# Kernel tuning notes

Measured on AMD Instinct MI355X. Metric: run time of the kernel, lower is better.

Reference implementation:

```python
import jax, jax.numpy as jnp
import numpy as np

H = 16  # num_attention_heads
D = 64  # attention_head_size


def setup_inputs() -> dict:
    key = jax.random.key(0)
    ks = jax.random.split(key, 10)
    B, S, Hid = 8, 512, 1024
    scale = 0.02
    hidden_states = jax.random.normal(ks[0], (B, S, Hid), jnp.float32)
    attention_mask = jnp.zeros((B, 1, 1, S), jnp.float32)
    graph_emb = jax.random.randint(ks[1], (B, S, S), 0, 3, jnp.int32)
    Wq = jax.random.normal(ks[2], (Hid, Hid), jnp.float32) * scale
    bq = jnp.zeros((Hid,), jnp.float32)
    Wk = jax.random.normal(ks[3], (Hid, Hid), jnp.float32) * scale
    bk = jnp.zeros((Hid,), jnp.float32)
    Wv = jax.random.normal(ks[4], (Hid, Hid), jnp.float32) * scale
    bv = jnp.zeros((Hid,), jnp.float32)
    dp_k = jax.random.normal(ks[5], (3, D), jnp.float32) * scale
    dp_v = jax.random.normal(ks[6], (3, D), jnp.float32) * scale
    return {"hidden_states": hidden_states, "attention_mask": attention_mask,
            "graph_emb": graph_emb, "Wq": Wq, "bq": bq, "Wk": Wk, "bk": bk,
            "Wv": Wv, "bv": bv, "dp_k": dp_k, "dp_v": dp_v}


def reference(hidden_states, attention_mask, graph_emb, Wq, bq, Wk, bk, Wv, bv, dp_k, dp_v):
    B, S, Hid = hidden_states.shape

    def proj(W, b):  # nn.Linear: x @ W.T + b, then split heads -> [B,H,S,D]
        y = hidden_states @ W.T + b
        return y.reshape(B, S, H, D).transpose(0, 2, 1, 3)

    q = proj(Wq, bq)
    k = proj(Wk, bk)
    v = proj(Wv, bv)

    # padding_idx=0 -> row 0 of relation tables is zero
    dp_k = dp_k.at[0].set(0.0)
    dp_v = dp_v.at[0].set(0.0)
    dp_keys = dp_k[graph_emb]    # [B,S,S,D]
    dp_values = dp_v[graph_emb]  # [B,S,S,D]

    scores = jnp.einsum('bhqd,bhkd->bhqk', q, k) / jnp.sqrt(jnp.float32(D))
    scores = scores + jnp.einsum('bhqd,bqkd->bhqk', q, dp_keys)  # relative_matmul_dp
    scores = scores + attention_mask
    probs = jax.nn.softmax(scores, axis=-1)

    ctx = jnp.einsum('bhqk,bhkd->bhqd', probs, v)
    ctx = ctx + jnp.einsum('bhqk,bqkd->bhqd', probs, dp_values)  # relative_matmul_dpv
    return ctx.transpose(0, 2, 1, 3).reshape(B, S, H * D)
```

## Files before the change

### kernel.cpp

```cpp
#include <hip/hip_runtime.h>
#include <hip/hip_bf16.h>
#include <cstddef>

#define B_  8
#define S_  512
#define HID 1024
#define H_  16
#define D_  64

typedef float f32x4 __attribute__((ext_vector_type(4)));
typedef _Float16 f16x8 __attribute__((ext_vector_type(8)));
typedef short s16x8 __attribute__((ext_vector_type(8)));
typedef unsigned short u16t;

__device__ __forceinline__ u16t f2h(float v) {
    return __builtin_bit_cast(u16t, (_Float16)v);
}

__device__ __forceinline__ void gll16(const u16t* g, u16t* l) {
    __builtin_amdgcn_global_load_lds(
        (const __attribute__((address_space(1))) unsigned int*)(const void*)g,
        (__attribute__((address_space(3))) unsigned int*)(void*)l, 16, 0, 0);
}

#define WAITV4() asm volatile("s_waitcnt vmcnt(4)" ::: "memory")
#define WAITV0() asm volatile("s_waitcnt vmcnt(0)" ::: "memory")

__global__ __launch_bounds__(256) void conv_all_kernel(
    const float* __restrict__ X,
    const float* __restrict__ Wq, const float* __restrict__ Wk,
    const float* __restrict__ Wv,
    u16t* __restrict__ Xh, u16t* __restrict__ Wh)
{
    const int nX4 = (B_ * S_ * HID) / 4;
    const int nW4 = (HID * HID) / 4;
    int i = blockIdx.x * 256 + threadIdx.x;
    const float* src;
    u16t* dst;
    int off;
    if (i < nX4)                { src = X;  dst = Xh;                         off = i; }
    else if (i < nX4 + nW4)     { src = Wq; dst = Wh;                         off = i - nX4; }
    else if (i < nX4 + 2 * nW4) { src = Wk; dst = Wh + (size_t)HID * HID;     off = i - nX4 - nW4; }
    else                        { src = Wv; dst = Wh + (size_t)2 * HID * HID; off = i - nX4 - 2 * nW4; }
    float4 x = ((const float4*)src)[off];
    ushort4 h;
    h.x = f2h(x.x);
    h.y = f2h(x.y);
    h.z = f2h(x.z);
    h.w = f2h(x.w);
    ((ushort4*)dst)[off] = h;
}

__global__ __launch_bounds__(256) void pack_ge_kernel(
    const int* __restrict__ ge, unsigned char* __restrict__ ge8, int n4)
{
    int i = blockIdx.x * 256 + threadIdx.x;
    if (i >= n4) return;
    int4 v = ((const int4*)ge)[i];
    uchar4 p;
    p.x = (unsigned char)v.x;
    p.y = (unsigned char)v.y;
    p.z = (unsigned char)v.z;
    p.w = (unsigned char)v.w;
    ((uchar4*)ge8)[i] = p;
}

__global__ __launch_bounds__(256) void qkv_mfma_kernel(
    const u16t* __restrict__ Xhi, const u16t* __restrict__ Whi,
    const float* __restrict__ bq, const float* __restrict__ bk,
    const float* __restrict__ bv,
    u16t* __restrict__ Qh, u16t* __restrict__ Kh, u16t* __restrict__ Vth)
{
    const int which = blockIdx.z;
    const u16t* __restrict__ WhiB = Whi + (size_t)which * (HID * HID);
    const float* __restrict__ bias = (which == 0) ? bq : (which == 1) ? bk : bv;

    __shared__ __align__(16) u16t SM[24576];

    const int tid  = threadIdx.x;
    const int lane = tid & 63;
    const int wv_  = tid >> 6;
    const int wr   = wv_ >> 1;
    const int wc   = wv_ & 1;
    const int m0   = blockIdx.y * 128;
    const int n0   = blockIdx.x * 128;
    const int NT   = HID / 32;

    f32x4 acc[4][4];
    #pragma unroll
    for (int mi = 0; mi < 4; ++mi)
        #pragma unroll
        for (int ni = 0; ni < 4; ++ni)
            #pragma unroll
            for (int e = 0; e < 4; ++e) acc[mi][ni][e] = 0.0f;

    const int c0 = tid, c1 = 256 + tid;
    const int rp0 = c0 >> 3, u0 = (c0 & 7) ^ (rp0 & 7);
    const int rp1 = c1 >> 3, u1 = (c1 & 7) ^ (rp1 & 7);
    const size_t ga0 = (size_t)(m0 + 2 * rp0 + (u0 >> 2)) * HID + (u0 & 3) * 8;
    const size_t ga1 = (size_t)(m0 + 2 * rp1 + (u1 >> 2)) * HID + (u1 & 3) * 8;
    const size_t gb0 = (size_t)(n0 + 2 * rp0 + (u0 >> 2)) * HID + (u0 & 3) * 8;
    const size_t gb1 = (size_t)(n0 + 2 * rp1 + (u1 >> 2)) * HID + (u1 & 3) * 8;
    const int lA0 = wv_ * 512;
    const int lA1 = 2048 + wv_ * 512;

    const int colL = lane & 15;
    const int kg   = lane >> 4;
    int aoffR[4], boffR[4];
    #pragma unroll
    for (int mi = 0; mi < 4; ++mi) {
        const int mrow = wr * 64 + mi * 16 + colL;
        const int rp = mrow >> 1, hf = mrow & 1;
        aoffR[mi] = rp * 64 + ((((hf << 2) | kg) ^ (rp & 7)) << 3);
        const int nrow = wc * 64 + mi * 16 + colL;
        const int rq = nrow >> 1, hg = nrow & 1;
        boffR[mi] = rq * 64 + ((((hg << 2) | kg) ^ (rq & 7)) << 3);
    }

    #define STAGE_T(t) do {                                      \
        u16t* bb_ = SM + ((t) % 3) * 8192;                       \
        const size_t ko_ = (size_t)(t) * 32;                     \
        gll16(&Xhi [ga0 + ko_], bb_ + lA0);                      \
        gll16(&Xhi [ga1 + ko_], bb_ + lA1);                      \
        gll16(&WhiB[gb0 + ko_], bb_ + 4096 + lA0);               \
        gll16(&WhiB[gb1 + ko_], bb_ + 4096 + lA1);               \
    } while (0)

    STAGE_T(0);
    STAGE_T(1);

    for (int t = 0; t < NT; ++t) {
        if (t < NT - 1) WAITV4();
        else            WAITV0();
        __builtin_amdgcn_s_barrier();
        if (t + 2 < NT) STAGE_T(t + 2);

        u16t* const bc = SM + (t % 3) * 8192;
        f16x8 a_[4], b_[4];
        #pragma unroll
        for (int mi = 0; mi < 4; ++mi)
            a_[mi] = *(const f16x8*)&bc[aoffR[mi]];
        #pragma unroll
        for (int ni = 0; ni < 4; ++ni)
            b_[ni] = *(const f16x8*)&bc[4096 + boffR[ni]];
        #pragma unroll
        for (int mi = 0; mi < 4; ++mi)
            #pragma unroll
            for (int ni = 0; ni < 4; ++ni)
                acc[mi][ni] = __builtin_amdgcn_mfma_f32_16x16x32_f16(
                    a_[mi], b_[ni], acc[mi][ni], 0, 0, 0);
    }
    #undef STAGE_T

    if (which == 2) {
        #pragma unroll
        for (int mi = 0; mi < 4; ++mi) {
            #pragma unroll
            for (int ni = 0; ni < 4; ++ni) {
                const int n    = n0 + wc * 64 + ni * 16 + colL;
                const int mrow = m0 + wr * 64 + mi * 16 + kg * 4;
                const float bn = bias[n];
                const int bb = mrow >> 9;
                const int ss = mrow & (S_ - 1);
                const int hh = n >> 6;
                const int dd = n & (D_ - 1);
                ushort4 vh;
                vh.x = f2h(acc[mi][ni][0] + bn);
                vh.y = f2h(acc[mi][ni][1] + bn);
                vh.z = f2h(acc[mi][ni][2] + bn);
                vh.w = f2h(acc[mi][ni][3] + bn);
                *(ushort4*)&Vth[(((size_t)bb * H_ + hh) * D_ + dd) * S_ + ss] = vh;
            }
        }
    } else {
        u16t* __restrict__ Oh = (which == 0) ? Qh : Kh;
        float* LF = (float*)SM;
        float bn4[4];
        #pragma unroll
        for (int ni = 0; ni < 4; ++ni) bn4[ni] = bias[n0 + wc * 64 + ni * 16 + colL];

        const int er  = tid >> 3;
        const int ecc = (tid & 7) * 16;
        const int ehh = (n0 + ecc) >> 6;
        const int edd = ecc & 63;
        const int mrowE = m0 + (er >> 4) * 64 + (er & 15);

        #pragma unroll
        for (int mi = 0; mi < 4; ++mi) {
            __syncthreads();
            #pragma unroll
            for (int ni = 0; ni < 4; ++ni)
                #pragma unroll
                for (int j = 0; j < 4; ++j)
                    LF[(wr * 16 + kg * 4 + j) * 130 + wc * 64 + ni * 16 + colL] =
                        acc[mi][ni][j] + bn4[ni];
            __syncthreads();

            const int mrow = mrowE + mi * 16;
            const int bb = mrow >> 9;
            const int ss = mrow & (S_ - 1);
            __align__(16) u16t hv[16];
            #pragma unroll
            for (int u = 0; u < 16; u += 4) {
                float4 v = *(const float4*)&LF[er * 130 + ecc + u];
                hv[u + 0] = f2h(v.x);
                hv[u + 1] = f2h(v.y);
                hv[u + 2] = f2h(v.z);
                hv[u + 3] = f2h(v.w);
            }
            const size_t off = (((size_t)bb * H_ + ehh) * S_ + ss) * D_ + edd;
            *(s16x8*)&Oh[off]     = *(const s16x8*)&hv[0];
            *(s16x8*)&Oh[off + 8] = *(const s16x8*)&hv[8];
        }
    }
}

__global__ __launch_bounds__(512) void attn_mfma_kernel(
    const u16t* __restrict__ Qhg, const u16t* __restrict__ Khg,
    const u16t* __restrict__ Vhg,
    const unsigned char* __restrict__ ge8, const float* __restrict__ mask,
    const float* __restrict__ dpk, const float* __restrict__ dpv,
    float* __restrict__ out)
{
    __shared__ __align__(16) u16t SM[24576];

    const int tid  = threadIdx.x;
    const int lane = tid & 63;
    const int wq   = tid >> 6;
    const int c    = lane & 15;
    const int g    = lane >> 4;
    const int sx   = c & 7;
    const int bid  = blockIdx.x;
    const int bh   = bid >> 2;
    const int q0   = (bid & 3) * 128;
    const int b    = bh >> 4;
    const int h    = bh & (H_ - 1);

    u16t* Pw = SM + 16384 + wq * 1024;

    const int qrow = q0 + wq * 16 + c;
    const size_t qoff = ((size_t)bh * S_ + qrow) * D_;
    const f16x8 qA = *(const f16x8*)&Qhg[qoff + g * 8];
    const f16x8 qB = *(const f16x8*)&Qhg[qoff + (g + 4) * 8];

    float tq1, tq2;
    {
        float a1 = 0.f, a2 = 0.f;
        #pragma unroll
        for (int i = 0; i < 8; ++i) {
            const float x0 = (float)qA[i];
            const float x1 = (float)qB[i];
            a1 = fmaf(x0, dpk[D_ + g * 8 + i], a1);
            a1 = fmaf(x1, dpk[D_ + (g + 4) * 8 + i], a1);
            a2 = fmaf(x0, dpk[2 * D_ + g * 8 + i], a2);
            a2 = fmaf(x1, dpk[2 * D_ + (g + 4) * 8 + i], a2);
        }
        a1 += __shfl_xor(a1, 16); a1 += __shfl_xor(a1, 32);
        a2 += __shfl_xor(a2, 16); a2 += __shfl_xor(a2, 32);
        tq1 = a1; tq2 = a2;
    }

    const int r_   = tid >> 3;
    const int s_   = tid & 7;
    const int ldso = r_ * 64 + ((s_ ^ (r_ & 7)) << 3);
    const u16t* kgp = &Khg[((size_t)bh * S_ + r_) * D_ + s_ * 8];
    const u16t* vgp = &Vhg[((size_t)bh * D_ + r_) * S_ + s_ * 8];

    s16x8 krS = *(const s16x8*)kgp;
    s16x8 vrS = *(const s16x8*)vgp;

    const size_t geoff = ((size_t)b * S_ + qrow) * S_;
    const float* mrow = &mask[(size_t)b * S_];

    float lrun = 0.f, w1 = 0.f, w2 = 0.f;
    f32x4 ctx4[4];
    #pragma unroll
    for (int mi = 0; mi < 4; ++mi)
        #pragma unroll
        for (int e = 0; e < 4; ++e) ctx4[mi][e] = 0.f;

    for (int kt = 0; kt < S_ / 64; ++kt) {
        const int k0 = kt * 64;
        const int bufo = (kt & 1) << 13;
        u16t* const Kb = SM + bufo;
        u16t* const Vb = SM + bufo + 4096;

        *(s16x8*)&Kb[ldso] = krS;
        *(s16x8*)&Vb[ldso] = vrS;

        if (kt < S_ / 64 - 1) {
            krS = *(const s16x8*)(kgp + (size_t)(k0 + 64) * D_);
            vrS = *(const s16x8*)(vgp + (k0 + 64));
        }
        uchar4 gc4[4];
        float4 mk4[4];
        #pragma unroll
        for (int mi = 0; mi < 4; ++mi) {
            gc4[mi] = *(const uchar4*)&ge8[geoff + k0 + mi * 16 + g * 4];
            mk4[mi] = *(const float4*)&mrow[k0 + mi * 16 + g * 4];
        }

        __syncthreads();

        f32x4 s4[4];
        #pragma unroll
        for (int mi = 0; mi < 4; ++mi)
            #pragma unroll
            for (int e = 0; e < 4; ++e) s4[mi][e] = 0.f;

        __builtin_amdgcn_s_setprio(1);
        #pragma unroll
        for (int ks = 0; ks < 2; ++ks) {
            const int so = ((g + 4 * ks) ^ sx) << 3;
            const f16x8 qh_ = ks ? qB : qA;
            #pragma unroll
            for (int mi = 0; mi < 4; ++mi) {
                const f16x8 kh_ = *(const f16x8*)&Kb[(mi * 16 + c) * 64 + so];
                s4[mi] = __builtin_amdgcn_mfma_f32_16x16x32_f16(kh_, qh_, s4[mi], 0, 0, 0);
            }
        }
        __builtin_amdgcn_s_setprio(0);

        float sv[4][4];
        float rs = 0.f, rb1 = 0.f, rb2 = 0.f;
        #pragma unroll
        for (int mi = 0; mi < 4; ++mi) {
            const int   gg[4] = {gc4[mi].x, gc4[mi].y, gc4[mi].z, gc4[mi].w};
            const float mm[4] = {mk4[mi].x, mk4[mi].y, mk4[mi].z, mk4[mi].w};
            #pragma unroll
            for (int j = 0; j < 4; ++j) {
                const float t = (gg[j] == 1) ? tq1 : (gg[j] == 2) ? tq2 : 0.f;
                const float e = __expf(fmaf(s4[mi][j], 0.125f, t + mm[j] - 8.0f));
                sv[mi][j] = e;
                rs += e;
                rb1 += (gg[j] == 1) ? e : 0.f;
                rb2 += (gg[j] == 2) ? e : 0.f;
            }
        }
        rs  += __shfl_xor(rs, 16);  rs  += __shfl_xor(rs, 32);
        rb1 += __shfl_xor(rb1, 16); rb1 += __shfl_xor(rb1, 32);
        rb2 += __shfl_xor(rb2, 16); rb2 += __shfl_xor(rb2, 32);
        lrun += rs;
        w1   += rb1;
        w2   += rb2;

        #pragma unroll
        for (int mi = 0; mi < 4; ++mi) {
            ushort4 ph;
            ph.x = f2h(sv[mi][0]);
            ph.y = f2h(sv[mi][1]);
            ph.z = f2h(sv[mi][2]);
            ph.w = f2h(sv[mi][3]);
            const int slotp = (2 * mi + (g >> 1)) ^ sx;
            *(ushort4*)&Pw[c * 64 + slotp * 8 + (g & 1) * 4] = ph;
        }

        __builtin_amdgcn_s_setprio(1);
        #pragma unroll
        for (int ks = 0; ks < 2; ++ks) {
            const int so = ((g + 4 * ks) ^ sx) << 3;
            const f16x8 ph_ = *(const f16x8*)&Pw[c * 64 + so];
            #pragma unroll
            for (int mi = 0; mi < 4; ++mi) {
                const f16x8 vh_ = *(const f16x8*)&Vb[(mi * 16 + c) * 64 + so];
                ctx4[mi] = __builtin_amdgcn_mfma_f32_16x16x32_f16(vh_, ph_, ctx4[mi], 0, 0, 0);
            }
        }
        __builtin_amdgcn_s_setprio(0);
    }

    __syncthreads();
    const float inv = 1.0f / lrun;
    float* tb = (float*)SM + wq * 1088;
    #pragma unroll
    for (int mi = 0; mi < 4; ++mi) {
        const float4 dk1 = *(const float4*)&dpv[D_ + mi * 16 + g * 4];
        const float4 dk2 = *(const float4*)&dpv[2 * D_ + mi * 16 + g * 4];
        const float a1[4] = {dk1.x, dk1.y, dk1.z, dk1.w};
        const float a2[4] = {dk2.x, dk2.y, dk2.z, dk2.w};
        #pragma unroll
        for (int j = 0; j < 4; ++j) {
            const float val = (ctx4[mi][j] + w1 * a1[j] + w2 * a2[j]) * inv;
            tb[(mi * 16 + g * 4 + j) * 17 + c] = val;
        }
    }
    __syncthreads();
    #pragma unroll
    for (int qq = 0; qq < 16; ++qq)
        out[((size_t)b * S_ + q0 + wq * 16 + qq) * (H_ * D_) + h * D_ + lane] =
            tb[lane * 17 + qq];
}

extern "C" void kernel_launch(void* const* d_in, const int* in_sizes, int n_in,
                              void* d_out, int out_size, void* d_ws, size_t ws_size,
                              hipStream_t stream)
{
    const float* hs   = (const float*)d_in[0];
    const float* mask = (const float*)d_in[1];
    const int*   ge   = (const int*)d_in[2];
    const float* Wq   = (const float*)d_in[3];
    const float* bq   = (const float*)d_in[4];
    const float* Wk   = (const float*)d_in[5];
    const float* bk   = (const float*)d_in[6];
    const float* Wv   = (const float*)d_in[7];
    const float* bv   = (const float*)d_in[8];
    const float* dpk  = (const float*)d_in[9];
    const float* dpv  = (const float*)d_in[10];
    float* out = (float*)d_out;

    const size_t per = (size_t)B_ * H_ * S_ * D_;
    const size_t nX  = (size_t)B_ * S_ * HID;
    const size_t nW  = (size_t)HID * HID;
    const size_t nGe = (size_t)B_ * S_ * S_;

    u16t* base = (u16t*)d_ws;
    u16t* Qh  = base;
    u16t* Kh  = Qh  + per;
    u16t* Vth = Kh  + per;
    u16t* Xhi = Vth + per;
    u16t* Whi = Xhi + nX;
    unsigned char* ge8 = (unsigned char*)(Whi + 3 * nW);

    const int nConv = (int)((nX + 3 * nW) / 4);
    conv_all_kernel<<<nConv / 256, 256, 0, stream>>>(hs, Wq, Wk, Wv, Xhi, Whi);
    pack_ge_kernel<<<(int)(nGe / 4 / 256), 256, 0, stream>>>(ge, ge8, (int)(nGe / 4));

    dim3 gridG(HID / 128, (B_ * S_) / 128, 3);
    qkv_mfma_kernel<<<gridG, dim3(256), 0, stream>>>(
        Xhi, Whi, bq, bk, bv, Qh, Kh, Vth);

    dim3 gridB(B_ * H_ * (S_ / 128));
    attn_mfma_kernel<<<gridB, dim3(512), 0, stream>>>(
        Qh, Kh, Vth, ge8, mask, dpk, dpv, out);
}
```

Measured before the change: 84.54 us.

## Fuse Q/K/V projections into one GEMM block and drop graph-emb packing kernel

The QKV projection kernel now computes all three projections in one block, staging the shared X tile once and three weight tiles per k-step. Three accumulator sets are kept, and the grid shrinks from 3 slices to 1. This reuses the X loads across Q, K and V, but it triples accumulator registers (launch bounds set to 1 block), doubles LDS use and leaves far fewer blocks (256) to fill the GPU. Separately, the int8 pack kernel for graph_emb is removed and the attention kernel reads the int32 indices directly, saving a launch and a pass at the cost of 4x wider index loads inside attention.

```diff
diff --git a/kernel.cpp b/kernel.cpp
--- a/kernel.cpp
+++ b/kernel.cpp
@@ -23,7 +23,7 @@
         (__attribute__((address_space(3))) unsigned int*)(void*)l, 16, 0, 0);
 }
 
-#define WAITV4() asm volatile("s_waitcnt vmcnt(4)" ::: "memory")
+#define WAITV8() asm volatile("s_waitcnt vmcnt(8)" ::: "memory")
 #define WAITV0() asm volatile("s_waitcnt vmcnt(0)" ::: "memory")
 
 __global__ __launch_bounds__(256) void conv_all_kernel(
@@ -51,31 +51,17 @@
     ((ushort4*)dst)[off] = h;
 }
 
-__global__ __launch_bounds__(256) void pack_ge_kernel(
-    const int* __restrict__ ge, unsigned char* __restrict__ ge8, int n4)
-{
-    int i = blockIdx.x * 256 + threadIdx.x;
-    if (i >= n4) return;
-    int4 v = ((const int4*)ge)[i];
-    uchar4 p;
-    p.x = (unsigned char)v.x;
-    p.y = (unsigned char)v.y;
-    p.z = (unsigned char)v.z;
-    p.w = (unsigned char)v.w;
-    ((uchar4*)ge8)[i] = p;
-}
-
-__global__ __launch_bounds__(256) void qkv_mfma_kernel(
+__global__ __launch_bounds__(256, 1) void qkv_mfma_kernel(
     const u16t* __restrict__ Xhi, const u16t* __restrict__ Whi,
     const float* __restrict__ bq, const float* __restrict__ bk,
     const float* __restrict__ bv,
     u16t* __restrict__ Qh, u16t* __restrict__ Kh, u16t* __restrict__ Vth)
 {
-    const int which = blockIdx.z;
-    const u16t* __restrict__ WhiB = Whi + (size_t)which * (HID * HID);
-    const float* __restrict__ bias = (which == 0) ? bq : (which == 1) ? bk : bv;
-
-    __shared__ __align__(16) u16t SM[24576];
+    const u16t* __restrict__ Wh0 = Whi;
+    const u16t* __restrict__ Wh1 = Whi + (size_t)(HID * HID);
+    const u16t* __restrict__ Wh2 = Whi + (size_t)2 * (HID * HID);
+
+    __shared__ __align__(16) u16t SM[49152];
 
     const int tid  = threadIdx.x;
     const int lane = tid & 63;
@@ -86,13 +72,15 @@
     const int n0   = blockIdx.x * 128;
     const int NT   = HID / 32;
 
-    f32x4 acc[4][4];
+    f32x4 acc[3][4][4];
     #pragma unroll
-    for (int mi = 0; mi < 4; ++mi)
-        #pragma unroll
-        for (int ni = 0; ni < 4; ++ni)
-            #pragma unroll
-            for (int e = 0; e < 4; ++e) acc[mi][ni][e] = 0.0f;
+    for (int w = 0; w < 3; ++w)
+        #pragma unroll
+        for (int mi = 0; mi < 4; ++mi)
+            #pragma unroll
+            for (int ni = 0; ni < 4; ++ni)
+                #pragma unroll
+                for (int e = 0; e < 4; ++e) acc[w][mi][ni][e] = 0.0f;
 
     const int c0 = tid, c1 = 256 + tid;
     const int rp0 = c0 >> 3, u0 = (c0 & 7) ^ (rp0 & 7);
@@ -118,99 +106,111 @@
     }
 
     #define STAGE_T(t) do {                                      \
-        u16t* bb_ = SM + ((t) % 3) * 8192;                       \
+        u16t* bb_ = SM + ((t) % 3) * 16384;                      \
         const size_t ko_ = (size_t)(t) * 32;                     \
-        gll16(&Xhi [ga0 + ko_], bb_ + lA0);                      \
-        gll16(&Xhi [ga1 + ko_], bb_ + lA1);                      \
-        gll16(&WhiB[gb0 + ko_], bb_ + 4096 + lA0);               \
-        gll16(&WhiB[gb1 + ko_], bb_ + 4096 + lA1);               \
+        gll16(&Xhi[ga0 + ko_], bb_ + lA0);                       \
+        gll16(&Xhi[ga1 + ko_], bb_ + lA1);                       \
+        gll16(&Wh0[gb0 + ko_], bb_ + 4096  + lA0);               \
+        gll16(&Wh0[gb1 + ko_], bb_ + 4096  + lA1);               \
+        gll16(&Wh1[gb0 + ko_], bb_ + 8192  + lA0);               \
+        gll16(&Wh1[gb1 + ko_], bb_ + 8192  + lA1);               \
+        gll16(&Wh2[gb0 + ko_], bb_ + 12288 + lA0);               \
+        gll16(&Wh2[gb1 + ko_], bb_ + 12288 + lA1);               \
     } while (0)
 
     STAGE_T(0);
     STAGE_T(1);
 
     for (int t = 0; t < NT; ++t) {
-        if (t < NT - 1) WAITV4();
+        if (t < NT - 1) WAITV8();
         else            WAITV0();
         __builtin_amdgcn_s_barrier();
         if (t + 2 < NT) STAGE_T(t + 2);
 
-        u16t* const bc = SM + (t % 3) * 8192;
-        f16x8 a_[4], b_[4];
+        u16t* const bc = SM + (t % 3) * 16384;
+        f16x8 a_[4];
         #pragma unroll
         for (int mi = 0; mi < 4; ++mi)
             a_[mi] = *(const f16x8*)&bc[aoffR[mi]];
         #pragma unroll
-        for (int ni = 0; ni < 4; ++ni)
-            b_[ni] = *(const f16x8*)&bc[4096 + boffR[ni]];
-        #pragma unroll
-        for (int mi = 0; mi < 4; ++mi)
+        for (int w = 0; w < 3; ++w) {
+            f16x8 b_[4];
             #pragma unroll
             for (int ni = 0; ni < 4; ++ni)
-                acc[mi][ni] = __builtin_amdgcn_mfma_f32_16x16x32_f16(
-                    a_[mi], b_[ni], acc[mi][ni], 0, 0, 0);
+                b_[ni] = *(const f16x8*)&bc[4096 * (w + 1) + boffR[ni]];
+            #pragma unroll
+            for (int mi = 0; mi < 4; ++mi)
+                #pragma unroll
+                for (int ni = 0; ni < 4; ++ni)
+                    acc[w][mi][ni] = __builtin_amdgcn_mfma_f32_16x16x32_f16(
+                        a_[mi], b_[ni], acc[w][mi][ni], 0, 0, 0);
+        }
     }
     #undef STAGE_T
 
-    if (which == 2) {
+    {
+        float* LF = (float*)SM;
+        const int er  = tid >> 3;
+        const int ecc = (tid & 7) * 16;
+        const int ehh = (n0 + ecc) >> 6;
+        const int edd = ecc & 63;
+        const int mrowE = m0 + (er >> 4) * 64 + (er & 15);
+
+        #pragma unroll
+        for (int w = 0; w < 2; ++w) {
+            const float* __restrict__ bias = (w == 0) ? bq : bk;
+            u16t* __restrict__ Oh = (w == 0) ? Qh : Kh;
+            float bn4[4];
+            #pragma unroll
+            for (int ni = 0; ni < 4; ++ni) bn4[ni] = bias[n0 + wc * 64 + ni * 16 + colL];
+
+            #pragma unroll
+            for (int mi = 0; mi < 4; ++mi) {
+                __syncthreads();
+                #pragma unroll
+                for (int ni = 0; ni < 4; ++ni)
+                    #pragma unroll
+                    for (int j = 0; j < 4; ++j)
+                        LF[(wr * 16 + kg * 4 + j) * 130 + wc * 64 + ni * 16 + colL] =
+                            acc[w][mi][ni][j] + bn4[ni];
+                __syncthreads();
+
+                const int mrow = mrowE + mi * 16;
+                const int bb = mrow >> 9;
+                const int ss = mrow & (S_ - 1);
+                __align__(16) u16t hv[16];
+                #pragma unroll
+                for (int u = 0; u < 16; u += 4) {
+                    float4 v = *(const float4*)&LF[er * 130 + ecc + u];
+                    hv[u + 0] = f2h(v.x);
+                    hv[u + 1] = f2h(v.y);
+                    hv[u + 2] = f2h(v.z);
+                    hv[u + 3] = f2h(v.w);
+                }
+                const size_t off = (((size_t)bb * H_ + ehh) * S_ + ss) * D_ + edd;
+                *(s16x8*)&Oh[off]     = *(const s16x8*)&hv[0];
+                *(s16x8*)&Oh[off + 8] = *(const s16x8*)&hv[8];
+            }
+        }
+
         #pragma unroll
         for (int mi = 0; mi < 4; ++mi) {
             #pragma unroll
             for (int ni = 0; ni < 4; ++ni) {
                 const int n    = n0 + wc * 64 + ni * 16 + colL;
                 const int mrow = m0 + wr * 64 + mi * 16 + kg * 4;
-                const float bn = bias[n];
+                const float bn = bv[n];
                 const int bb = mrow >> 9;
                 const int ss = mrow & (S_ - 1);
                 const int hh = n >> 6;
                 const int dd = n & (D_ - 1);
                 ushort4 vh;
-                vh.x = f2h(acc[mi][ni][0] + bn);
-                vh.y = f2h(acc[mi][ni][1] + bn);
-                vh.z = f2h(acc[mi][ni][2] + bn);
-                vh.w = f2h(acc[mi][ni][3] + bn);
+                vh.x = f2h(acc[2][mi][ni][0] + bn);
+                vh.y = f2h(acc[2][mi][ni][1] + bn);
+                vh.z = f2h(acc[2][mi][ni][2] + bn);
+                vh.w = f2h(acc[2][mi][ni][3] + bn);
                 *(ushort4*)&Vth[(((size_t)bb * H_ + hh) * D_ + dd) * S_ + ss] = vh;
             }
-        }
-    } else {
-        u16t* __restrict__ Oh = (which == 0) ? Qh : Kh;
-        float* LF = (float*)SM;
-        float bn4[4];
-        #pragma unroll
-        for (int ni = 0; ni < 4; ++ni) bn4[ni] = bias[n0 + wc * 64 + ni * 16 + colL];
-
-        const int er  = tid >> 3;
-        const int ecc = (tid & 7) * 16;
-        const int ehh = (n0 + ecc) >> 6;
-        const int edd = ecc & 63;
-        const int mrowE = m0 + (er >> 4) * 64 + (er & 15);
-
-        #pragma unroll
-        for (int mi = 0; mi < 4; ++mi) {
-            __syncthreads();
-            #pragma unroll
-            for (int ni = 0; ni < 4; ++ni)
-                #pragma unroll
-                for (int j = 0; j < 4; ++j)
-                    LF[(wr * 16 + kg * 4 + j) * 130 + wc * 64 + ni * 16 + colL] =
-                        acc[mi][ni][j] + bn4[ni];
-            __syncthreads();
-
-            const int mrow = mrowE + mi * 16;
-            const int bb = mrow >> 9;
-            const int ss = mrow & (S_ - 1);
-            __align__(16) u16t hv[16];
-            #pragma unroll
-            for (int u = 0; u < 16; u += 4) {
-                float4 v = *(const float4*)&LF[er * 130 + ecc + u];
-                hv[u + 0] = f2h(v.x);
-                hv[u + 1] = f2h(v.y);
-                hv[u + 2] = f2h(v.z);
-                hv[u + 3] = f2h(v.w);
-            }
-            const size_t off = (((size_t)bb * H_ + ehh) * S_ + ss) * D_ + edd;
-            *(s16x8*)&Oh[off]     = *(const s16x8*)&hv[0];
-            *(s16x8*)&Oh[off + 8] = *(const s16x8*)&hv[8];
         }
     }
 }
@@ -218,7 +218,7 @@
 __global__ __launch_bounds__(512) void attn_mfma_kernel(
     const u16t* __restrict__ Qhg, const u16t* __restrict__ Khg,
     const u16t* __restrict__ Vhg,
-    const unsigned char* __restrict__ ge8, const float* __restrict__ mask,
+    const int*  __restrict__ ge,  const float* __restrict__ mask,
     const float* __restrict__ dpk, const float* __restrict__ dpv,
     float* __restrict__ out)
 {
@@ -292,11 +292,11 @@
             krS = *(const s16x8*)(kgp + (size_t)(k0 + 64) * D_);
             vrS = *(const s16x8*)(vgp + (k0 + 64));
         }
-        uchar4 gc4[4];
+        int4   gc4[4];
         float4 mk4[4];
         #pragma unroll
         for (int mi = 0; mi < 4; ++mi) {
-            gc4[mi] = *(const uchar4*)&ge8[geoff + k0 + mi * 16 + g * 4];
+            gc4[mi] = *(const int4*)&ge[geoff + k0 + mi * 16 + g * 4];
             mk4[mi] = *(const float4*)&mrow[k0 + mi * 16 + g * 4];
         }
 
@@ -411,7 +411,6 @@
     const size_t per = (size_t)B_ * H_ * S_ * D_;
     const size_t nX  = (size_t)B_ * S_ * HID;
     const size_t nW  = (size_t)HID * HID;
-    const size_t nGe = (size_t)B_ * S_ * S_;
 
     u16t* base = (u16t*)d_ws;
     u16t* Qh  = base;
@@ -419,17 +418,15 @@
     u16t* Vth = Kh  + per;
     u16t* Xhi = Vth + per;
     u16t* Whi = Xhi + nX;
-    unsigned char* ge8 = (unsigned char*)(Whi + 3 * nW);
 
     const int nConv = (int)((nX + 3 * nW) / 4);
     conv_all_kernel<<<nConv / 256, 256, 0, stream>>>(hs, Wq, Wk, Wv, Xhi, Whi);
-    pack_ge_kernel<<<(int)(nGe / 4 / 256), 256, 0, stream>>>(ge, ge8, (int)(nGe / 4));
-
-    dim3 gridG(HID / 128, (B_ * S_) / 128, 3);
+
+    dim3 gridG(HID / 128, (B_ * S_) / 128);
     qkv_mfma_kernel<<<gridG, dim3(256), 0, stream>>>(
         Xhi, Whi, bq, bk, bv, Qh, Kh, Vth);
 
     dim3 gridB(B_ * H_ * (S_ / 128));
     attn_mfma_kernel<<<gridB, dim3(512), 0, stream>>>(
-        Qh, Kh, Vth, ge8, mask, dpk, dpv, out);
-}
+        Qh, Kh, Vth, ge, mask, dpk, dpv, out);
+}
```

After: 81.60 us. 3.5% less time.
